# Kernel tuning notes

Hardware: AMD Instinct MI355X
Metric: run time of the kernel (lower is better)

The kernel has to match this reference:

```python
import jax, jax.numpy as jnp
import numpy as np

NUM_HEADS = 16


def setup_inputs() -> dict:
    key = jax.random.key(0)
    k1, k2, k3 = jax.random.split(key, 3)
    B, N, C = 4, 2048, 1024
    x = jax.random.normal(k1, (B, N, C), dtype=jnp.float32)
    w_qkv = jax.random.normal(k2, (C, 3 * C), dtype=jnp.float32) * (C ** -0.5)
    w_proj = jax.random.normal(k3, (C, C), dtype=jnp.float32) * (C ** -0.5)
    b_proj = jnp.zeros((C,), dtype=jnp.float32)
    return {"x": x, "w_qkv": w_qkv, "w_proj": w_proj, "b_proj": b_proj}


def reference(x, w_qkv, w_proj, b_proj):
    B, N, C = x.shape
    H = NUM_HEADS
    hd = C // H
    scale = hd ** -0.5
    # qkv projection (no bias), split into q, k, v per head
    qkv = jnp.einsum('bnc,cd->bnd', x, w_qkv)            # [B, N, 3C]
    qkv = qkv.reshape(B, N, 3, H, hd).transpose(0, 3, 2, 1, 4)  # [B, H, 3, N, hd]
    q, k, v = qkv[:, :, 0], qkv[:, :, 1], qkv[:, :, 2]   # each [B, H, N, hd]
    q = q * scale
    attn = jax.nn.softmax(jnp.einsum('bhnd,bhmd->bhnm', q, k), axis=-1)  # [B, H, N, N]
    out = jnp.einsum('bhnm,bhmd->bhnd', attn, v)         # [B, H, N, hd]
    out = out.transpose(0, 2, 1, 3).reshape(B, N, C)
    return jnp.einsum('bnc,cd->bnd', out, w_proj) + b_proj
```

## Files before the change

kernel.cpp:

```cpp
#include <hip/hip_runtime.h>

typedef short s16x8 __attribute__((ext_vector_type(8)));
typedef float f32x4 __attribute__((ext_vector_type(4)));
typedef float f32x16 __attribute__((ext_vector_type(16)));
typedef unsigned u32x4 __attribute__((ext_vector_type(4)));


__device__ __forceinline__ unsigned short bf16bits(float f) {
  unsigned u = __builtin_bit_cast(unsigned, f);
  unsigned rnd = 0x7FFFu + ((u >> 16) & 1u);
  return (unsigned short)((u + rnd) >> 16);
}

__device__ __forceinline__ unsigned pk_bf16(float lo, float hi) {
  unsigned r;
  asm("v_cvt_pk_bf16_f32 %0, %1, %2" : "=v"(r) : "v"(lo), "v"(hi));
  return r;
}

__device__ __forceinline__ void async16(const void* g, void* l) {
  __builtin_amdgcn_global_load_lds((const __attribute__((address_space(1))) void*)g,
                                   (__attribute__((address_space(3))) void*)l, 16, 0, 0);
}

__device__ __forceinline__ f32x4 mfma16(s16x8 a, s16x8 b, f32x4 c) {
  return __builtin_amdgcn_mfma_f32_16x16x32_bf16(a, b, c, 0, 0, 0);
}

__device__ __forceinline__ f32x16 mfma32(s16x8 a, s16x8 b, f32x16 c) {
  return __builtin_amdgcn_mfma_f32_32x32x16_bf16(a, b, c, 0, 0, 0);
}

__device__ __forceinline__ s16x8 lds_frag(const unsigned short* S, int row, int c8, int U) {
  int unit = row * U + (c8 ^ (row & (U - 1)));
  return *(const s16x8*)(S + unit * 8);
}


__global__ __launch_bounds__(256) void cvt_f32_bf16(const float4* __restrict__ in,
                                                    unsigned short* __restrict__ out, int n4) {
  int i = blockIdx.x * blockDim.x + threadIdx.x;
  int stride = gridDim.x * blockDim.x;
  for (; i < n4; i += stride) {
    float4 v = in[i];
    uint2 o;
    o.x = pk_bf16(v.x, v.y);
    o.y = pk_bf16(v.z, v.w);
    *(uint2*)(out + (size_t)i * 4) = o;
  }
}

__global__ __launch_bounds__(256) void transpose_f32_bf16(const float* __restrict__ in,
                                                          unsigned short* __restrict__ out,
                                                          int R, int C) {
  __shared__ float tile[32][33];
  int c0 = blockIdx.x * 32, r0 = blockIdx.y * 32;
  int tx = threadIdx.x, ty = threadIdx.y;
  #pragma unroll
  for (int i = 0; i < 32; i += 8)
    tile[ty + i][tx] = in[(size_t)(r0 + ty + i) * C + c0 + tx];
  __syncthreads();
  #pragma unroll
  for (int i = 0; i < 32; i += 8)
    out[(size_t)(c0 + ty + i) * R + r0 + tx] = bf16bits(tile[tx][ty + i]);
}

__global__ __launch_bounds__(256) void transpose_v(const unsigned short* __restrict__ V,
                                                   unsigned short* __restrict__ Vt) {
  __shared__ unsigned short sm[64 * 68];
  int bh = blockIdx.y, kt0 = blockIdx.x * 64;
  const unsigned short* v = V + (size_t)bh * 2048 * 64 + (size_t)kt0 * 64;
  unsigned short* vt = Vt + (size_t)bh * 64 * 2048;
  int t = threadIdx.x;
  #pragma unroll
  for (int i = 0; i < 4; ++i) {
    int u = i * 256 + t;
    int f = u * 4;
    int k = f >> 6, d0 = f & 63;
    *(uint2*)&sm[k * 68 + d0] = *(const uint2*)&v[f];
  }
  __syncthreads();
  #pragma unroll
  for (int j = 0; j < 16; ++j) {
    int o = j * 256 + t;
    int d = o >> 6, k = o & 63;
    vt[(size_t)d * 2048 + kt0 + k] = sm[k * 68 + d];
  }
}


template <typename EPI>
__global__ __launch_bounds__(512, 2) void gemm8(const unsigned short* __restrict__ A,
                                                const unsigned short* __restrict__ Bt,
                                                int K, EPI epi) {
  __shared__ __align__(16) unsigned short As[3 * 128 * 64];
  __shared__ __align__(16) unsigned short Bs[3 * 256 * 64];
  const int tid = threadIdx.x, wid = tid >> 6, lane = tid & 63;
  const int quad = lane >> 4, l16 = lane & 15;
  const int bm0 = blockIdx.y * 128, bn0 = blockIdx.x * 256;
  const int wm = (wid & 1) * 64, wn = (wid >> 1) * 64;
  const int NT = K >> 6;
  f32x4 acc[4][4] = {};

  const int srow = tid >> 3;
  const int sc8 = (tid & 7) ^ (srow & 7);
  auto stage = [&](int b, int tk, int k) {
    int col = tk * 64 + sc8 * 8;
    if (k < 2)
      async16(A + (size_t)(bm0 + k * 64 + srow) * K + col,
              (char*)As + b * 16384 + k * 8192 + wid * 1024);
    else
      async16(Bt + (size_t)(bn0 + (k - 2) * 64 + srow) * K + col,
              (char*)Bs + b * 32768 + (k - 2) * 8192 + wid * 1024);
  };

  #pragma unroll
  for (int k = 0; k < 6; ++k) stage(0, 0, k);
  #pragma unroll
  for (int k = 0; k < 6; ++k) stage(1, 1, k);

  int bc = 0;
  for (int t = 0; t < NT; ++t) {
    const unsigned short* as = As + bc * 8192;
    const unsigned short* bs = Bs + bc * 16384;
    const int bp = (bc == 0) ? 2 : bc - 1;

    if (t + 2 < NT) {
      stage(bp, t + 2, 0); stage(bp, t + 2, 1); stage(bp, t + 2, 2);
      asm volatile("s_waitcnt vmcnt(9)" ::: "memory");
    } else if (t + 1 < NT) {
      asm volatile("s_waitcnt vmcnt(6)" ::: "memory");
    } else {
      asm volatile("s_waitcnt vmcnt(0)" ::: "memory");
    }
    __builtin_amdgcn_s_barrier();
    __builtin_amdgcn_sched_barrier(0);

    #pragma unroll
    for (int kk = 0; kk < 2; ++kk) {
      s16x8 a[4], b[4];
      #pragma unroll
      for (int i = 0; i < 4; ++i) a[i] = lds_frag(as, wm + i * 16 + l16, kk * 4 + quad, 8);
      #pragma unroll
      for (int j = 0; j < 4; ++j) b[j] = lds_frag(bs, wn + j * 16 + l16, kk * 4 + quad, 8);
      if (kk == 0 && t + 2 < NT) {
        stage(bp, t + 2, 3); stage(bp, t + 2, 4); stage(bp, t + 2, 5);
      }
      __builtin_amdgcn_s_setprio(1);
      #pragma unroll
      for (int i = 0; i < 4; ++i)
        #pragma unroll
        for (int j = 0; j < 4; ++j)
          acc[i][j] = mfma16(a[i], b[j], acc[i][j]);
      __builtin_amdgcn_s_setprio(0);
    }
    __builtin_amdgcn_sched_barrier(0);
    __builtin_amdgcn_s_barrier();
    bc = (bc == 2) ? 0 : bc + 1;
  }

  #pragma unroll
  for (int i = 0; i < 4; ++i)
    #pragma unroll
    for (int j = 0; j < 4; ++j)
      epi.store4(bm0 + wm + i * 16 + quad * 4, bn0 + wn + j * 16 + l16, acc[i][j]);
}

struct QKVEpi {
  unsigned short *Q, *K, *V;
  float qscale;
  __device__ __forceinline__ void store4(int m0, int n, f32x4 v) const {
    int s = m0 >> 10, h = (m0 >> 6) & 15, d = m0 & 63;
    int b = n >> 11, ns = n & 2047;
    unsigned short* dst = (s == 0) ? Q : ((s == 1) ? K : V);
    float sc = (s == 0) ? qscale : 1.f;
    uint2 o;
    o.x = pk_bf16(v[0] * sc, v[1] * sc);
    o.y = pk_bf16(v[2] * sc, v[3] * sc);
    *(uint2*)&dst[(((size_t)b * 16 + h) * 2048 + ns) * 64 + d] = o;
  }
};

struct ProjEpi {
  const float* bias;
  float* out;
  __device__ __forceinline__ void store4(int m0, int n, f32x4 v) const {
    float4 b4 = *(const float4*)&bias[m0];
    float4 o = {v[0] + b4.x, v[1] + b4.y, v[2] + b4.z, v[3] + b4.w};
    *(float4*)&out[(size_t)n * 1024 + m0] = o;
  }
};

__global__ __launch_bounds__(256, 4) void flash_attn(const unsigned short* __restrict__ Q,
                                                     const unsigned short* __restrict__ K,
                                                     const unsigned short* __restrict__ Vt,
                                                     unsigned short* __restrict__ O) {
  __shared__ __align__(16) unsigned short Ks[2][8 * 512];
  __shared__ __align__(16) unsigned short Vs[2][8 * 512];
  const int tid = threadIdx.x, wid = tid >> 6, lane = tid & 63;
  const int l31 = lane & 31, half = lane >> 5;
  const int bid = blockIdx.y * gridDim.x + blockIdx.x;
  const int xcd = bid & 7, idx = bid >> 3;
  const int bh = xcd * 8 + (idx & 7);
  const int qt = idx >> 3;
  const unsigned short* Qg = Q + (size_t)bh * 2048 * 64;
  const unsigned short* Kg = K + (size_t)bh * 2048 * 64;
  const unsigned short* Vg = Vt + (size_t)bh * 64 * 2048;
  const int qrow = qt * 128 + wid * 32 + l31;

  s16x8 qB[4];
  #pragma unroll
  for (int s = 0; s < 4; ++s)
    qB[s] = *(const s16x8*)&Qg[(size_t)qrow * 64 + s * 16 + half * 8];

  const bool isK = wid < 2;
  int sA[4];
  #pragma unroll
  for (int t = 0; t < 4; ++t) {
    int c = (wid & 1) * 4 + t;
    if (isK) sA[t] = ((c >> 2) * 32 + l31) * 64 + ((c & 3) * 2 + half) * 8;
    else     sA[t] = ((c & 1) * 32 + l31) * 2048 + (c >> 1) * 16 + half * 8;
  }

  auto stage = [&](int kt, int buf) {
    const int kb = kt * 64;
    #pragma unroll
    for (int t = 0; t < 4; ++t) {
      int c = (wid & 1) * 4 + t;
      if (isK) async16(Kg + (size_t)kb * 64 + sA[t], (char*)&Ks[buf][0] + c * 1024);
      else     async16(Vg + kb + sA[t],              (char*)&Vs[buf][0] + c * 1024);
    }
  };

  f32x16 oacc[2] = {};
  float l_i = 0.f;
  const f32x16 fz = {};

  stage(0, 0);
  for (int kt = 0; kt < 32; ++kt) {
    const int cur = kt & 1;
    __syncthreads();
    if (kt + 1 < 32) stage(kt + 1, cur ^ 1);
    const unsigned short* ks = &Ks[cur][0];
    const unsigned short* vs = &Vs[cur][0];

    #pragma unroll
    for (int kf = 0; kf < 2; ++kf) {
      f32x16 st;
      __builtin_amdgcn_s_setprio(1);
      {
        s16x8 a = *(const s16x8*)&ks[((kf * 4 + 0) * 64 + lane) * 8];
        st = mfma32(a, qB[0], fz);
      }
      #pragma unroll
      for (int s = 1; s < 4; ++s) {
        s16x8 a = *(const s16x8*)&ks[((kf * 4 + s) * 64 + lane) * 8];
        st = mfma32(a, qB[s], st);
      }
      __builtin_amdgcn_s_setprio(0);
      float a0 = 0.f, a1 = 0.f, a2 = 0.f, a3 = 0.f;
      #pragma unroll
      for (int r = 0; r < 16; r += 4) {
        float p0 = __builtin_amdgcn_exp2f(st[r + 0]);
        float p1 = __builtin_amdgcn_exp2f(st[r + 1]);
        float p2 = __builtin_amdgcn_exp2f(st[r + 2]);
        float p3 = __builtin_amdgcn_exp2f(st[r + 3]);
        st[r + 0] = p0; st[r + 1] = p1; st[r + 2] = p2; st[r + 3] = p3;
        a0 += p0; a1 += p1; a2 += p2; a3 += p3;
      }
      float rs = (a0 + a1) + (a2 + a3);
      rs += __shfl_xor(rs, 32);
      l_i += rs;
      #pragma unroll
      for (int t = 0; t < 2; ++t) {
        int rb = t * 8;
        unsigned pa0 = pk_bf16(st[rb + 0], st[rb + 1]);
        unsigned pa1 = pk_bf16(st[rb + 2], st[rb + 3]);
        unsigned pb0 = pk_bf16(st[rb + 4], st[rb + 5]);
        unsigned pb1 = pk_bf16(st[rb + 6], st[rb + 7]);
        unsigned s0 = half ? pa0 : pb0;
        unsigned s1 = half ? pa1 : pb1;
        unsigned r0 = (unsigned)__shfl_xor((int)s0, 32);
        unsigned r1 = (unsigned)__shfl_xor((int)s1, 32);
        u32x4 bP;
        bP[0] = half ? r0 : pa0;
        bP[1] = half ? r1 : pa1;
        bP[2] = half ? pb0 : r0;
        bP[3] = half ? pb1 : r1;
        __builtin_amdgcn_s_setprio(1);
        #pragma unroll
        for (int f = 0; f < 2; ++f) {
          s16x8 aV = *(const s16x8*)&vs[(((kf * 2 + t) * 2 + f) * 64 + lane) * 8];
          oacc[f] = mfma32(aV, __builtin_bit_cast(s16x8, bP), oacc[f]);
        }
        __builtin_amdgcn_s_setprio(0);
      }
    }
  }

  const int b = bh >> 4, h = bh & 15;
  float inv = 1.f / l_i;
  size_t base = (((size_t)b * 2048 + qrow) * 16 + h) * 64;
  #pragma unroll
  for (int f = 0; f < 2; ++f)
    #pragma unroll
    for (int q = 0; q < 4; ++q) {
      int d0 = f * 32 + q * 8 + half * 4;
      uint2 o;
      o.x = pk_bf16(oacc[f][q * 4 + 0] * inv, oacc[f][q * 4 + 1] * inv);
      o.y = pk_bf16(oacc[f][q * 4 + 2] * inv, oacc[f][q * 4 + 3] * inv);
      *(uint2*)&O[base + d0] = o;
    }
}


extern "C" void kernel_launch(void* const* d_in, const int* in_sizes, int n_in,
                              void* d_out, int out_size, void* d_ws, size_t ws_size,
                              hipStream_t stream) {
  (void)in_sizes; (void)n_in; (void)out_size; (void)ws_size;
  const float* x = (const float*)d_in[0];
  const float* w_qkv = (const float*)d_in[1];
  const float* w_proj = (const float*)d_in[2];
  const float* b_proj = (const float*)d_in[3];
  float* out = (float*)d_out;
  char* ws = (char*)d_ws;
  const size_t MB = 1ull << 20;
  unsigned short* Xb  = (unsigned short*)(ws);
  unsigned short* Wqt = (unsigned short*)(ws + 16 * MB);
  unsigned short* Wpt = (unsigned short*)(ws + 22 * MB);
  unsigned short* Qb  = (unsigned short*)(ws + 24 * MB);
  unsigned short* Kb  = (unsigned short*)(ws + 40 * MB);
  unsigned short* Vb  = (unsigned short*)(ws + 56 * MB);
  unsigned short* Vt  = Xb;
  unsigned short* Ob  = Vb;

  cvt_f32_bf16<<<2048, 256, 0, stream>>>((const float4*)x, Xb, 8388608 / 4);
  transpose_f32_bf16<<<dim3(96, 32), dim3(32, 8), 0, stream>>>(w_qkv, Wqt, 1024, 3072);
  transpose_f32_bf16<<<dim3(32, 32), dim3(32, 8), 0, stream>>>(w_proj, Wpt, 1024, 1024);

  QKVEpi e1{Qb, Kb, Vb, 0.125f * 1.44269504088896340736f};
  gemm8<QKVEpi><<<dim3(32, 24), 512, 0, stream>>>(Wqt, Xb, 1024, e1);

  transpose_v<<<dim3(32, 64), 256, 0, stream>>>(Vb, Vt);
  flash_attn<<<dim3(16, 64), 256, 0, stream>>>(Qb, Kb, Vt, Ob);

  ProjEpi e2{b_proj, out};
  gemm8<ProjEpi><<<dim3(32, 8), 512, 0, stream>>>(Wpt, Ob, 1024, e2);
}
```

Measured before the change: 295.0 us.

## Restructure GEMM prefetch pipeline with split staging and per-half barriers

Reworks the triple-buffered GEMM main loop. The wait for the next tile moves to the end of each iteration, and the first wait is hoisted before the loop. Prefetch of tile t+2 is split evenly across the two k-halves, with a barrier around each MFMA block. The goal is to keep the memory loads more evenly overlapped with MFMA work and remove the stall at the top of each iteration. The cost is extra workgroup barriers per iteration.

New measurement: 276.7 us. 6.2% less time.

```diff
diff --git a/kernel.cpp b/kernel.cpp
--- a/kernel.cpp
+++ b/kernel.cpp
@@ -104,37 +104,30 @@
 
   const int srow = tid >> 3;
   const int sc8 = (tid & 7) ^ (srow & 7);
-  auto stage = [&](int b, int tk, int k) {
+  auto stage = [&](int s, int tk, int k) {
     int col = tk * 64 + sc8 * 8;
     if (k < 2)
       async16(A + (size_t)(bm0 + k * 64 + srow) * K + col,
-              (char*)As + b * 16384 + k * 8192 + wid * 1024);
+              (char*)As + s * 16384 + k * 8192 + wid * 1024);
     else
       async16(Bt + (size_t)(bn0 + (k - 2) * 64 + srow) * K + col,
-              (char*)Bs + b * 32768 + (k - 2) * 8192 + wid * 1024);
+              (char*)Bs + s * 32768 + (k - 2) * 8192 + wid * 1024);
   };
 
   #pragma unroll
   for (int k = 0; k < 6; ++k) stage(0, 0, k);
   #pragma unroll
   for (int k = 0; k < 6; ++k) stage(1, 1, k);
-
-  int bc = 0;
+  asm volatile("s_waitcnt vmcnt(6)" ::: "memory");
+  __builtin_amdgcn_s_barrier();
+  __builtin_amdgcn_sched_barrier(0);
+
+  int sc = 0;
   for (int t = 0; t < NT; ++t) {
-    const unsigned short* as = As + bc * 8192;
-    const unsigned short* bs = Bs + bc * 16384;
-    const int bp = (bc == 0) ? 2 : bc - 1;
-
-    if (t + 2 < NT) {
-      stage(bp, t + 2, 0); stage(bp, t + 2, 1); stage(bp, t + 2, 2);
-      asm volatile("s_waitcnt vmcnt(9)" ::: "memory");
-    } else if (t + 1 < NT) {
-      asm volatile("s_waitcnt vmcnt(6)" ::: "memory");
-    } else {
-      asm volatile("s_waitcnt vmcnt(0)" ::: "memory");
-    }
-    __builtin_amdgcn_s_barrier();
-    __builtin_amdgcn_sched_barrier(0);
+    const unsigned short* as = As + sc * 8192;
+    const unsigned short* bs = Bs + sc * 16384;
+    const int sp = (sc == 0) ? 2 : sc - 1;
+    const bool pf = (t + 2 < NT);
 
     #pragma unroll
     for (int kk = 0; kk < 2; ++kk) {
@@ -143,9 +136,9 @@
       for (int i = 0; i < 4; ++i) a[i] = lds_frag(as, wm + i * 16 + l16, kk * 4 + quad, 8);
       #pragma unroll
       for (int j = 0; j < 4; ++j) b[j] = lds_frag(bs, wn + j * 16 + l16, kk * 4 + quad, 8);
-      if (kk == 0 && t + 2 < NT) {
-        stage(bp, t + 2, 3); stage(bp, t + 2, 4); stage(bp, t + 2, 5);
-      }
+      if (pf) { stage(sp, t + 2, kk * 3 + 0); stage(sp, t + 2, kk * 3 + 1); stage(sp, t + 2, kk * 3 + 2); }
+      __builtin_amdgcn_sched_barrier(0);
+      __builtin_amdgcn_s_barrier();
       __builtin_amdgcn_s_setprio(1);
       #pragma unroll
       for (int i = 0; i < 4; ++i)
@@ -153,10 +146,14 @@
         for (int j = 0; j < 4; ++j)
           acc[i][j] = mfma16(a[i], b[j], acc[i][j]);
       __builtin_amdgcn_s_setprio(0);
+      __builtin_amdgcn_sched_barrier(0);
+      if (kk == 1) {
+        if (pf) asm volatile("s_waitcnt vmcnt(6)" ::: "memory");
+        else    asm volatile("s_waitcnt vmcnt(0)" ::: "memory");
+      }
+      __builtin_amdgcn_s_barrier();
     }
-    __builtin_amdgcn_sched_barrier(0);
-    __builtin_amdgcn_s_barrier();
-    bc = (bc == 2) ? 0 : bc + 1;
+    sc = (sc == 2) ? 0 : sc + 1;
   }
 
   #pragma unroll
```
